# Kernel tuning notes

Hardware: AMD Instinct MI355X
Metric: run time of the kernel (lower is better)

## Reference

```python
import jax, jax.numpy as jnp
import numpy as np

START, STOP, T = 28, 29, 30

def _lstm_dir(x, h0, c0, w_ih, w_hh, b_ih, b_hh):
    # x: (S, B, E) -> hs: (S, B, H)
    xw = jnp.einsum('sbe,ge->sbg', x, w_ih) + b_ih + b_hh  # (S,B,4H)
    def step(carry, g_x):
        h, c = carry
        g = g_x + h @ w_hh.T
        i, f, gg, o = jnp.split(g, 4, axis=-1)
        c = jax.nn.sigmoid(f) * c + jax.nn.sigmoid(i) * jnp.tanh(gg)
        h = jax.nn.sigmoid(o) * jnp.tanh(c)
        return (h, c), h
    _, hs = jax.lax.scan(step, (h0, c0), xw)
    return hs

def setup_inputs() -> dict:
    key = jax.random.key(0)
    ks = jax.random.split(key, 16)
    S, B, V, E, H = 256, 32, 50000, 512, 512  # H = hidden_dim // 2
    d = {}
    d['sentence'] = jax.random.randint(ks[0], (S, B), 0, V)
    d['tags'] = jax.random.randint(ks[1], (S, B), 0, 28)
    d['emb'] = jax.random.normal(ks[2], (V, E), jnp.float32) * 0.1
    d['w_ih_f'] = jax.random.normal(ks[3], (4 * H, E), jnp.float32) * 0.05
    d['w_hh_f'] = jax.random.normal(ks[4], (4 * H, H), jnp.float32) * 0.05
    d['b_ih_f'] = jax.random.normal(ks[5], (4 * H,), jnp.float32) * 0.05
    d['b_hh_f'] = jax.random.normal(ks[6], (4 * H,), jnp.float32) * 0.05
    d['w_ih_b'] = jax.random.normal(ks[7], (4 * H, E), jnp.float32) * 0.05
    d['w_hh_b'] = jax.random.normal(ks[8], (4 * H, H), jnp.float32) * 0.05
    d['b_ih_b'] = jax.random.normal(ks[9], (4 * H,), jnp.float32) * 0.05
    d['b_hh_b'] = jax.random.normal(ks[10], (4 * H,), jnp.float32) * 0.05
    d['w_out'] = jax.random.normal(ks[11], (T, 2 * H), jnp.float32) * 0.05
    d['b_out'] = jax.random.normal(ks[12], (T,), jnp.float32) * 0.05
    tr = jax.random.normal(ks[13], (T, T), jnp.float32)
    tr = tr.at[START, :].set(-10000.0).at[:, STOP].set(-10000.0)
    d['transitions'] = tr
    d['h0'] = jax.random.normal(ks[14], (2, B, H), jnp.float32)
    d['c0'] = jax.random.normal(ks[15], (2, B, H), jnp.float32)
    return d

def reference(sentence, tags, emb, w_ih_f, w_hh_f, b_ih_f, b_hh_f,
              w_ih_b, w_hh_b, b_ih_b, b_hh_b, w_out, b_out, transitions, h0, c0):
    S, B = sentence.shape
    x = emb[sentence]                                   # (S,B,E)
    hf = _lstm_dir(x, h0[0], c0[0], w_ih_f, w_hh_f, b_ih_f, b_hh_f)
    hb = _lstm_dir(x[::-1], h0[1], c0[1], w_ih_b, w_hh_b, b_ih_b, b_hh_b)[::-1]
    lstm_out = jnp.concatenate([hf, hb], axis=-1)       # (S,B,2H)
    feats = jnp.einsum('sbh,th->bst', lstm_out, w_out) + b_out  # (B,S,T)

    # CRF partition function (forward algorithm)
    fv0 = jnp.full((B, T), -10000.0, feats.dtype).at[:, START].set(0.0)
    def crf_step(fv, feat):  # fv (B,T), feat (B,T)
        fv = jax.nn.logsumexp(fv[:, None, :] + transitions[None, :, :] + feat[:, :, None], axis=2)
        return fv, None
    fv, _ = jax.lax.scan(crf_step, fv0, feats.transpose(1, 0, 2))
    forward_score = jax.nn.logsumexp(fv + transitions[STOP][None, :], axis=1)  # (B,)

    # gold path score
    tags_b = tags.T                                     # (B,S)
    tags_ext = jnp.concatenate([jnp.full((B, 1), START, tags_b.dtype), tags_b], axis=1)  # (B,S+1)
    t_prev, t_next = tags_ext[:, :-1], tags_ext[:, 1:]
    trans_sc = transitions[t_next, t_prev].sum(axis=1)
    emit_sc = jnp.take_along_axis(feats, t_next[:, :, None], axis=2)[:, :, 0].sum(axis=1)
    gold_score = trans_sc + emit_sc + transitions[STOP, tags_ext[:, -1]]

    return jnp.sum(forward_score - gold_score)
```

## Files before the change

### kernel.cpp

```cpp
#include <hip/hip_runtime.h>
#include <hip/hip_bf16.h>
#include <math.h>

#define S_LEN 256
#define B 32
#define E 512
#define H 512
#define G4 2048
#define T_TAGS 30
#define START_TAG 28
#define STOP_TAG 29

typedef unsigned short u16;
typedef unsigned int   u32;
typedef unsigned long long u64;
typedef __attribute__((ext_vector_type(8))) short bf16x8;
typedef __attribute__((ext_vector_type(4))) float f32x4;

__device__ __forceinline__ float bf2f(u16 u){
  u32 x = ((u32)u) << 16;
  return __uint_as_float(x);
}
__device__ __forceinline__ u16 f2bf(float f){
  u32 x = __float_as_uint(f);
  u32 r = (x + 0x7fffu + ((x >> 16) & 1u)) >> 16;
  return (u16)r;
}
__device__ __forceinline__ float sigf(float x){
  return 1.0f / (1.0f + __expf(-x));
}
__device__ __forceinline__ float tanh_fast(float x){
  return 1.0f - 2.0f / (__expf(2.0f * x) + 1.0f);
}

__global__ __launch_bounds__(256) void k_prep_a(
    const int* __restrict__ sent, const float* __restrict__ emb,
    u16* __restrict__ a16)
{
  int g = (blockIdx.x * 256 + threadIdx.x) * 8;
  int token = g >> 9, k = g & 511;
  const float* src = emb + (size_t)sent[token] * E + k;
  float4 v0 = *reinterpret_cast<const float4*>(src);
  float4 v1 = *reinterpret_cast<const float4*>(src + 4);
  u16 o[8];
  o[0]=f2bf(v0.x); o[1]=f2bf(v0.y); o[2]=f2bf(v0.z); o[3]=f2bf(v0.w);
  o[4]=f2bf(v1.x); o[5]=f2bf(v1.y); o[6]=f2bf(v1.z); o[7]=f2bf(v1.w);
  *reinterpret_cast<uint4*>(a16 + g) = *reinterpret_cast<const uint4*>(o);
}

__global__ __launch_bounds__(256) void k_cvt(const float* __restrict__ src, u16* __restrict__ dst){
  int g = (blockIdx.x * 256 + threadIdx.x) * 8;
  float4 v0 = *reinterpret_cast<const float4*>(src + g);
  float4 v1 = *reinterpret_cast<const float4*>(src + g + 4);
  u16 o[8];
  o[0]=f2bf(v0.x); o[1]=f2bf(v0.y); o[2]=f2bf(v0.z); o[3]=f2bf(v0.w);
  o[4]=f2bf(v1.x); o[5]=f2bf(v1.y); o[6]=f2bf(v1.z); o[7]=f2bf(v1.w);
  *reinterpret_cast<uint4*>(dst + g) = *reinterpret_cast<const uint4*>(o);
}

__global__ __launch_bounds__(256) void k_init16(
    const float* __restrict__ h0, u16* __restrict__ h16, u32* __restrict__ bar)
{
  int g = (blockIdx.x * 256 + threadIdx.x) * 8;
  float4 v0 = *reinterpret_cast<const float4*>(h0 + g);
  float4 v1 = *reinterpret_cast<const float4*>(h0 + g + 4);
  u16 o[8];
  o[0]=f2bf(v0.x); o[1]=f2bf(v0.y); o[2]=f2bf(v0.z); o[3]=f2bf(v0.w);
  o[4]=f2bf(v1.x); o[5]=f2bf(v1.y); o[6]=f2bf(v1.z); o[7]=f2bf(v1.w);
  *reinterpret_cast<uint4*>(h16 + g) = *reinterpret_cast<const uint4*>(o);
  if (blockIdx.x == 0 && threadIdx.x < 64) bar[threadIdx.x] = 0u;
}

__global__ __launch_bounds__(256) void k_gemm_xw16(
    const u16* __restrict__ a16, const u16* __restrict__ w16ih,
    const float* __restrict__ b_ih_f, const float* __restrict__ b_hh_f,
    const float* __restrict__ b_ih_b, const float* __restrict__ b_hh_b,
    u16* __restrict__ xw)
{
  int dir = blockIdx.z;
  int n0 = blockIdx.x * 128;
  int m0 = blockIdx.y * 128;
  const u16* Wp = w16ih + (size_t)dir * G4 * E;
  const float* bi = dir ? b_ih_b : b_ih_f;
  const float* bh = dir ? b_hh_b : b_hh_f;
  int tid = threadIdx.x;

  __shared__ u16 As[128 * 32];
  __shared__ u16 Bs[128 * 32];

  int l  = tid & 63;
  int wid = tid >> 6;
  int wr = wid >> 1, wc = wid & 1;
  int lr = l & 15, lh = l >> 4;
  int swzr = (lh ^ (lr & 3)) << 3;

  f32x4 acc[4][4];
  #pragma unroll
  for (int i = 0; i < 4; ++i)
    #pragma unroll
    for (int j = 0; j < 4; ++j)
      acc[i][j] = (f32x4){0.f, 0.f, 0.f, 0.f};

  for (int kt = 0; kt < E; kt += 32){
    __syncthreads();
    #pragma unroll
    for (int it = 0; it < 2; ++it){
      int u = it * 256 + tid;
      int row = u >> 2, c = u & 3;
      int sw = (c ^ (row & 3)) << 3;
      *reinterpret_cast<uint4*>(&As[row * 32 + sw]) =
        *reinterpret_cast<const uint4*>(a16 + (size_t)(m0 + row) * E + kt + c * 8);
      *reinterpret_cast<uint4*>(&Bs[row * 32 + sw]) =
        *reinterpret_cast<const uint4*>(Wp + (size_t)(n0 + row) * E + kt + c * 8);
    }
    __syncthreads();
    bf16x8 a[4], b[4];
    #pragma unroll
    for (int mi = 0; mi < 4; ++mi)
      a[mi] = *reinterpret_cast<const bf16x8*>(&As[(wr * 64 + mi * 16 + lr) * 32 + swzr]);
    #pragma unroll
    for (int ni = 0; ni < 4; ++ni)
      b[ni] = *reinterpret_cast<const bf16x8*>(&Bs[(wc * 64 + ni * 16 + lr) * 32 + swzr]);
    #pragma unroll
    for (int mi = 0; mi < 4; ++mi)
      #pragma unroll
      for (int ni = 0; ni < 4; ++ni)
        acc[mi][ni] = __builtin_amdgcn_mfma_f32_16x16x32_bf16(a[mi], b[ni], acc[mi][ni], 0, 0, 0);
  }

  #pragma unroll
  for (int ni = 0; ni < 4; ++ni){
    int n = n0 + wc * 64 + ni * 16 + lr;
    float bias = bi[n] + bh[n];
    #pragma unroll
    for (int mi = 0; mi < 4; ++mi){
      #pragma unroll
      for (int r = 0; r < 4; ++r){
        int m = m0 + wr * 64 + mi * 16 + lh * 4 + r;
        xw[((size_t)dir * 8192 + m) * G4 + n] = f2bf(acc[mi][ni][r] + bias);
      }
    }
  }
}

__global__ __launch_bounds__(128) void k_lstm_fast(
    const float* __restrict__ w_hh_f, const float* __restrict__ w_hh_b,
    const u16* __restrict__ xw,
    u16* __restrict__ ht,
    const float* __restrict__ c0,
    u16* __restrict__ hseq,
    u32* __restrict__ bar)
{
  __shared__ u16 w_s[64 * 512];

  const int bx    = blockIdx.x;
  const int dir   = bx >> 5;
  const int slice = bx & 31;
  const int j0    = slice << 4;
  const int tid   = threadIdx.x;
  const int l     = tid & 63;
  const int wr    = tid >> 6;
  const int lr    = l & 15, lh = l >> 4;
  const int sw    = (lr & 7) << 3;

  const float* wsrc = dir ? w_hh_b : w_hh_f;
  #pragma unroll
  for (int i = 0; i < 32; ++i){
    int u = i * 128 + tid;
    int r = u >> 6, ku8 = u & 63;
    int g = r >> 4, jj = r & 15;
    const float* src = wsrc + (size_t)((g << 9) + j0 + jj) * H + ku8 * 8;
    float4 a = *reinterpret_cast<const float4*>(src);
    float4 b = *reinterpret_cast<const float4*>(src + 4);
    u16 o[8];
    o[0]=f2bf(a.x); o[1]=f2bf(a.y); o[2]=f2bf(a.z); o[3]=f2bf(a.w);
    o[4]=f2bf(b.x); o[5]=f2bf(b.y); o[6]=f2bf(b.z); o[7]=f2bf(b.w);
    int idx = (r * 512 + ku8 * 8) ^ ((r & 7) << 3);
    *reinterpret_cast<uint4*>(&w_s[idx]) = *reinterpret_cast<const uint4*>(o);
  }

  int bbase[4];
  #pragma unroll
  for (int G = 0; G < 4; ++G)
    bbase[G] = (G * 16 + lr) * 512 + (lh << 3);

  const int aoff = ((wr << 4) + lr) * 512 + (lh << 3);

  float c_reg[4];
  #pragma unroll
  for (int r = 0; r < 4; ++r)
    c_reg[r] = c0[((size_t)dir * B + (wr * 16 + lh * 4 + r)) * H + j0 + lr];

  const u32* flg = bar + (dir << 5);
  const int PSTRIDE = 2 * B * H;

  __syncthreads();

  for (int t = 0; t < S_LEN; ++t){
    const int s_eff = dir ? (S_LEN - 1 - t) : t;

    u16 xv[4][4];
    {
      const u16* xb = xw + ((size_t)dir * 8192 + (size_t)s_eff * B) * G4 + j0 + lr;
      #pragma unroll
      for (int r = 0; r < 4; ++r){
        const u16* xr = xb + (size_t)(wr * 16 + lh * 4 + r) * G4;
        #pragma unroll
        for (int G = 0; G < 4; ++G) xv[G][r] = xr[G << 9];
      }
    }

    {
      u32 f;
      do {
        f = __hip_atomic_load(flg + (l & 31), __ATOMIC_RELAXED, __HIP_MEMORY_SCOPE_AGENT);
      } while (__any(f < (u32)t));
    }

    const u64* hp = reinterpret_cast<const u64*>(
        ht + (size_t)(t & 1) * PSTRIDE + (size_t)dir * (B * H) + aoff);
    u64 qa[32];
    #pragma unroll
    for (int kt = 0; kt < 16; ++kt){
      qa[2*kt]   = __hip_atomic_load(hp + kt * 8,     __ATOMIC_RELAXED, __HIP_MEMORY_SCOPE_AGENT);
      qa[2*kt+1] = __hip_atomic_load(hp + kt * 8 + 1, __ATOMIC_RELAXED, __HIP_MEMORY_SCOPE_AGENT);
    }

    f32x4 acc[4];
    #pragma unroll
    for (int G = 0; G < 4; ++G) acc[G] = (f32x4){0.f, 0.f, 0.f, 0.f};
    #pragma unroll
    for (int kt = 0; kt < 16; ++kt){
      union { u64 q[2]; bf16x8 v; } ua;
      ua.q[0] = qa[2*kt]; ua.q[1] = qa[2*kt+1];
      #pragma unroll
      for (int G = 0; G < 4; ++G){
        bf16x8 bfr = *reinterpret_cast<const bf16x8*>(&w_s[(bbase[G] + (kt << 5)) ^ sw]);
        acc[G] = __builtin_amdgcn_mfma_f32_16x16x32_bf16(ua.v, bfr, acc[G], 0, 0, 0);
      }
    }

    u32 spack[4];
    #pragma unroll
    for (int r = 0; r < 4; ++r){
      float iv = acc[0][r] + bf2f(xv[0][r]);
      float fv = acc[1][r] + bf2f(xv[1][r]);
      float gv = acc[2][r] + bf2f(xv[2][r]);
      float ov = acc[3][r] + bf2f(xv[3][r]);
      float cn = sigf(fv) * c_reg[r] + sigf(iv) * tanh_fast(gv);
      float hv = sigf(ov) * tanh_fast(cn);
      c_reg[r] = cn;
      u32 hu = (u32)f2bf(hv);
      u32 po = (u32)__shfl_xor((int)hu, 1);
      u32 pack = hu | (po << 16);
      spack[r] = pack;
      if ((lr & 1) == 0){
        int batch = wr * 16 + lh * 4 + r;
        size_t off = ((size_t)dir * B + batch) * H + j0 + lr;
        __hip_atomic_store(
            reinterpret_cast<u32*>(ht + (size_t)((t + 1) & 1) * PSTRIDE + off),
            pack, __ATOMIC_RELAXED, __HIP_MEMORY_SCOPE_AGENT);
      }
    }

    asm volatile("s_waitcnt vmcnt(0)" ::: "memory");
    __syncthreads();
    if (tid == 0)
      __hip_atomic_store(bar + (dir << 5) + slice, (u32)(t + 1),
                         __ATOMIC_RELAXED, __HIP_MEMORY_SCOPE_AGENT);

    if ((lr & 1) == 0){
      #pragma unroll
      for (int r = 0; r < 4; ++r){
        int batch = wr * 16 + lh * 4 + r;
        *reinterpret_cast<u32*>(
            hseq + ((size_t)dir * 8192 + (size_t)s_eff * B + batch) * H + j0 + lr) = spack[r];
      }
    }
  }
}

__global__ __launch_bounds__(256) void k_feats2(
    const u16* __restrict__ hseq, const float* __restrict__ w_out,
    const float* __restrict__ b_out, float* __restrict__ feats)
{
  __shared__ float row[32][1028];
  int blk = blockIdx.x;
  int tid = threadIdx.x;
  const u16* hf16 = hseq;
  const u16* hb16 = hseq + (size_t)8192 * H;

  #pragma unroll
  for (int it = 0; it < 16; ++it){
    int u = it * 256 + tid;
    int flat = u * 8;
    int i = flat >> 10, d = flat & 1023;
    int m = blk * 32 + i;
    const u16* src = (d < 512) ? (hf16 + (size_t)m * H + d) : (hb16 + (size_t)m * H + d - 512);
    uint4 v = *reinterpret_cast<const uint4*>(src);
    float* dst = &row[i][d];
    dst[0] = bf2f((u16)(v.x & 0xffff)); dst[1] = bf2f((u16)(v.x >> 16));
    dst[2] = bf2f((u16)(v.y & 0xffff)); dst[3] = bf2f((u16)(v.y >> 16));
    dst[4] = bf2f((u16)(v.z & 0xffff)); dst[5] = bf2f((u16)(v.z >> 16));
    dst[6] = bf2f((u16)(v.w & 0xffff)); dst[7] = bf2f((u16)(v.w >> 16));
  }
  __syncthreads();

  int i = tid >> 3, tg = tid & 7;
  const float* w0 = w_out + (size_t)((tg + 0  < T_TAGS) ? tg + 0  : 0) * 1024;
  const float* w1 = w_out + (size_t)((tg + 8  < T_TAGS) ? tg + 8  : 0) * 1024;
  const float* w2 = w_out + (size_t)((tg + 16 < T_TAGS) ? tg + 16 : 0) * 1024;
  const float* w3 = w_out + (size_t)((tg + 24 < T_TAGS) ? tg + 24 : 0) * 1024;
  float s0 = 0.f, s1 = 0.f, s2 = 0.f, s3 = 0.f;
  #pragma unroll 4
  for (int k4 = 0; k4 < 256; ++k4){
    float4 rv = *reinterpret_cast<const float4*>(&row[i][k4 * 4]);
    float4 a = *reinterpret_cast<const float4*>(w0 + k4 * 4);
    float4 b = *reinterpret_cast<const float4*>(w1 + k4 * 4);
    float4 c = *reinterpret_cast<const float4*>(w2 + k4 * 4);
    float4 d = *reinterpret_cast<const float4*>(w3 + k4 * 4);
    s0 = fmaf(a.x,rv.x,s0); s0 = fmaf(a.y,rv.y,s0); s0 = fmaf(a.z,rv.z,s0); s0 = fmaf(a.w,rv.w,s0);
    s1 = fmaf(b.x,rv.x,s1); s1 = fmaf(b.y,rv.y,s1); s1 = fmaf(b.z,rv.z,s1); s1 = fmaf(b.w,rv.w,s1);
    s2 = fmaf(c.x,rv.x,s2); s2 = fmaf(c.y,rv.y,s2); s2 = fmaf(c.z,rv.z,s2); s2 = fmaf(c.w,rv.w,s2);
    s3 = fmaf(d.x,rv.x,s3); s3 = fmaf(d.y,rv.y,s3); s3 = fmaf(d.z,rv.z,s3); s3 = fmaf(d.w,rv.w,s3);
  }
  int m = blk * 32 + i;
  int s = m >> 5, bb = m & 31;
  float* fp = feats + ((size_t)bb * S_LEN + s) * T_TAGS;
  float sums[4] = {s0, s1, s2, s3};
  #pragma unroll
  for (int q = 0; q < 4; ++q){
    int tt = tg + q * 8;
    if (tt < T_TAGS) fp[tt] = sums[q] + b_out[tt];
  }
}

__global__ __launch_bounds__(64) void k_crf2(
    const float* __restrict__ feats, const float* __restrict__ trans,
    const int* __restrict__ tags, float* __restrict__ scores)
{
  int b = blockIdx.x;
  int l = threadIdx.x;

  float trr[T_TAGS];
  #pragma unroll
  for (int j = 0; j < T_TAGS; ++j)
    trr[j] = (l < T_TAGS) ? trans[l * T_TAGS + j] : -1e30f;

  float fv = (l == START_TAG) ? 0.f : -10000.f;
  const float* fb = feats + (size_t)b * S_LEN * T_TAGS;

  for (int s = 0; s < S_LEN; ++s){
    float feat = (l < T_TAGS) ? fb[s * T_TAGS + l] : 0.f;
    float v[T_TAGS];
    float m = -1e30f;
    #pragma unroll
    for (int j = 0; j < T_TAGS; ++j){
      float fvj = __shfl(fv, j);
      v[j] = fvj + trr[j];
      m = fmaxf(m, v[j]);
    }
    float sum = 0.f;
    #pragma unroll
    for (int j = 0; j < T_TAGS; ++j) sum += __expf(v[j] - m);
    fv = feat + m + __logf(sum);
  }

  float fin = (l < T_TAGS) ? fv + trans[STOP_TAG * T_TAGS + l] : -1e30f;
  float mm = fin;
  #pragma unroll
  for (int o = 32; o > 0; o >>= 1) mm = fmaxf(mm, __shfl_xor(mm, o));
  float e = (l < T_TAGS) ? __expf(fin - mm) : 0.f;
  #pragma unroll
  for (int o = 32; o > 0; o >>= 1) e += __shfl_xor(e, o);
  float fsc = mm + __logf(e);

  float g = 0.f;
  #pragma unroll
  for (int it = 0; it < 4; ++it){
    int s = it * 64 + l;
    int nxt = tags[s * B + b];
    int prv = s ? tags[(s - 1) * B + b] : START_TAG;
    g += trans[nxt * T_TAGS + prv] + fb[s * T_TAGS + nxt];
  }
  #pragma unroll
  for (int o = 32; o > 0; o >>= 1) g += __shfl_down(g, o);
  if (l == 0){
    int last = tags[(S_LEN - 1) * B + b];
    g += trans[STOP_TAG * T_TAGS + last];
    scores[b] = fsc - g;
  }
}

__global__ void k_final(const float* __restrict__ scores, float* __restrict__ out){
  int tid = threadIdx.x;
  float v = (tid < B) ? scores[tid] : 0.f;
  #pragma unroll
  for (int o = 32; o > 0; o >>= 1) v += __shfl_down(v, o);
  if (tid == 0) out[0] = v;
}

extern "C" void kernel_launch(void* const* d_in, const int* in_sizes, int n_in,
                              void* d_out, int out_size, void* d_ws, size_t ws_size,
                              hipStream_t stream)
{
  const int*   sent   = (const int*)d_in[0];
  const int*   tags   = (const int*)d_in[1];
  const float* emb    = (const float*)d_in[2];
  const float* w_ih_f = (const float*)d_in[3];
  const float* w_hh_f = (const float*)d_in[4];
  const float* b_ih_f = (const float*)d_in[5];
  const float* b_hh_f = (const float*)d_in[6];
  const float* w_ih_b = (const float*)d_in[7];
  const float* w_hh_b = (const float*)d_in[8];
  const float* b_ih_b = (const float*)d_in[9];
  const float* b_hh_b = (const float*)d_in[10];
  const float* w_out  = (const float*)d_in[11];
  const float* b_out  = (const float*)d_in[12];
  const float* trans  = (const float*)d_in[13];
  const float* h0     = (const float*)d_in[14];
  const float* c0     = (const float*)d_in[15];

  const size_t OFF_XW   = 0;
  const size_t OFF_A16  = 67108864;
  const size_t OFF_WIH  = 75497472;
  const size_t OFF_HSEQ = 79691776;
  const size_t OFF_HT   = 96468992;
  const size_t OFF_FEATS= 96600064;
  const size_t OFF_SC   = 97583104;
  const size_t OFF_BAR  = 97583232;
  const size_t NEED     = 97583488;
  if (ws_size < NEED) return;

  char* ws = (char*)d_ws;
  u16*   xw     = (u16*)(ws + OFF_XW);
  u16*   a16    = (u16*)(ws + OFF_A16);
  u16*   w16ih  = (u16*)(ws + OFF_WIH);
  u16*   hseq   = (u16*)(ws + OFF_HSEQ);
  u16*   ht     = (u16*)(ws + OFF_HT);
  float* feats  = (float*)(ws + OFF_FEATS);
  float* scores = (float*)(ws + OFF_SC);
  u32*   bar    = (u32*)(ws + OFF_BAR);

  k_prep_a<<<2048, 256, 0, stream>>>(sent, emb, a16);
  k_cvt<<<512, 256, 0, stream>>>(w_ih_f, w16ih);
  k_cvt<<<512, 256, 0, stream>>>(w_ih_b, w16ih + (size_t)G4 * E);
  k_init16<<<16, 256, 0, stream>>>(h0, ht, bar);

  k_gemm_xw16<<<dim3(G4 / 128, 8192 / 128, 2), 256, 0, stream>>>(
      a16, w16ih, b_ih_f, b_hh_f, b_ih_b, b_hh_b, xw);

  k_lstm_fast<<<64, 128, 0, stream>>>(w_hh_f, w_hh_b, xw, ht, c0, hseq, bar);

  k_feats2<<<256, 256, 0, stream>>>(hseq, w_out, b_out, feats);
  k_crf2<<<B, 64, 0, stream>>>(feats, trans, tags, scores);
  k_final<<<1, 64, 0, stream>>>(scores, (float*)d_out);
}
```

Before: 1.604 ms.

## Fuse input projection GEMM into the persistent LSTM recurrence kernel

Removes the standalone bf16 input-projection GEMM and the two weight-conversion kernels. Each persistent LSTM block now keeps its slice of W_ih in LDS next to W_hh and computes the next timestep's x·W_ih with MFMAs right after publishing h. That step's accumulator then seeds the recurrent matmul, and the bias is added in the epilogue. This drops the large xw intermediate (write plus per-step strided reads) and its launch. The cost is extra MFMA work and global A loads inside the serial step loop, plus doubled LDS use per block.

```diff
diff --git a/kernel.cpp b/kernel.cpp
--- a/kernel.cpp
+++ b/kernel.cpp
@@ -48,16 +48,6 @@
   *reinterpret_cast<uint4*>(a16 + g) = *reinterpret_cast<const uint4*>(o);
 }
 
-__global__ __launch_bounds__(256) void k_cvt(const float* __restrict__ src, u16* __restrict__ dst){
-  int g = (blockIdx.x * 256 + threadIdx.x) * 8;
-  float4 v0 = *reinterpret_cast<const float4*>(src + g);
-  float4 v1 = *reinterpret_cast<const float4*>(src + g + 4);
-  u16 o[8];
-  o[0]=f2bf(v0.x); o[1]=f2bf(v0.y); o[2]=f2bf(v0.z); o[3]=f2bf(v0.w);
-  o[4]=f2bf(v1.x); o[5]=f2bf(v1.y); o[6]=f2bf(v1.z); o[7]=f2bf(v1.w);
-  *reinterpret_cast<uint4*>(dst + g) = *reinterpret_cast<const uint4*>(o);
-}
-
 __global__ __launch_bounds__(256) void k_init16(
     const float* __restrict__ h0, u16* __restrict__ h16, u32* __restrict__ bar)
 {
@@ -71,87 +61,43 @@
   if (blockIdx.x == 0 && threadIdx.x < 64) bar[threadIdx.x] = 0u;
 }
 
-__global__ __launch_bounds__(256) void k_gemm_xw16(
-    const u16* __restrict__ a16, const u16* __restrict__ w16ih,
+__device__ __forceinline__ void compute_xw(
+    const u64* __restrict__ ap, const u16* __restrict__ wih_s,
+    const int* __restrict__ bbase, int sw, f32x4* __restrict__ xacc)
+{
+  u64 qb[32];
+  #pragma unroll
+  for (int kt = 0; kt < 16; ++kt){
+    qb[2*kt]   = ap[kt * 8];
+    qb[2*kt+1] = ap[kt * 8 + 1];
+  }
+  #pragma unroll
+  for (int G = 0; G < 4; ++G) xacc[G] = (f32x4){0.f, 0.f, 0.f, 0.f};
+  #pragma unroll
+  for (int kt = 0; kt < 16; ++kt){
+    union { u64 q[2]; bf16x8 v; } ua;
+    ua.q[0] = qb[2*kt]; ua.q[1] = qb[2*kt+1];
+    #pragma unroll
+    for (int G = 0; G < 4; ++G){
+      bf16x8 bfr = *reinterpret_cast<const bf16x8*>(&wih_s[(bbase[G] + (kt << 5)) ^ sw]);
+      xacc[G] = __builtin_amdgcn_mfma_f32_16x16x32_bf16(ua.v, bfr, xacc[G], 0, 0, 0);
+    }
+  }
+}
+
+__global__ __launch_bounds__(128) void k_lstm_fused(
+    const float* __restrict__ w_hh_f, const float* __restrict__ w_hh_b,
+    const float* __restrict__ w_ih_f, const float* __restrict__ w_ih_b,
     const float* __restrict__ b_ih_f, const float* __restrict__ b_hh_f,
     const float* __restrict__ b_ih_b, const float* __restrict__ b_hh_b,
-    u16* __restrict__ xw)
-{
-  int dir = blockIdx.z;
-  int n0 = blockIdx.x * 128;
-  int m0 = blockIdx.y * 128;
-  const u16* Wp = w16ih + (size_t)dir * G4 * E;
-  const float* bi = dir ? b_ih_b : b_ih_f;
-  const float* bh = dir ? b_hh_b : b_hh_f;
-  int tid = threadIdx.x;
-
-  __shared__ u16 As[128 * 32];
-  __shared__ u16 Bs[128 * 32];
-
-  int l  = tid & 63;
-  int wid = tid >> 6;
-  int wr = wid >> 1, wc = wid & 1;
-  int lr = l & 15, lh = l >> 4;
-  int swzr = (lh ^ (lr & 3)) << 3;
-
-  f32x4 acc[4][4];
-  #pragma unroll
-  for (int i = 0; i < 4; ++i)
-    #pragma unroll
-    for (int j = 0; j < 4; ++j)
-      acc[i][j] = (f32x4){0.f, 0.f, 0.f, 0.f};
-
-  for (int kt = 0; kt < E; kt += 32){
-    __syncthreads();
-    #pragma unroll
-    for (int it = 0; it < 2; ++it){
-      int u = it * 256 + tid;
-      int row = u >> 2, c = u & 3;
-      int sw = (c ^ (row & 3)) << 3;
-      *reinterpret_cast<uint4*>(&As[row * 32 + sw]) =
-        *reinterpret_cast<const uint4*>(a16 + (size_t)(m0 + row) * E + kt + c * 8);
-      *reinterpret_cast<uint4*>(&Bs[row * 32 + sw]) =
-        *reinterpret_cast<const uint4*>(Wp + (size_t)(n0 + row) * E + kt + c * 8);
-    }
-    __syncthreads();
-    bf16x8 a[4], b[4];
-    #pragma unroll
-    for (int mi = 0; mi < 4; ++mi)
-      a[mi] = *reinterpret_cast<const bf16x8*>(&As[(wr * 64 + mi * 16 + lr) * 32 + swzr]);
-    #pragma unroll
-    for (int ni = 0; ni < 4; ++ni)
-      b[ni] = *reinterpret_cast<const bf16x8*>(&Bs[(wc * 64 + ni * 16 + lr) * 32 + swzr]);
-    #pragma unroll
-    for (int mi = 0; mi < 4; ++mi)
-      #pragma unroll
-      for (int ni = 0; ni < 4; ++ni)
-        acc[mi][ni] = __builtin_amdgcn_mfma_f32_16x16x32_bf16(a[mi], b[ni], acc[mi][ni], 0, 0, 0);
-  }
-
-  #pragma unroll
-  for (int ni = 0; ni < 4; ++ni){
-    int n = n0 + wc * 64 + ni * 16 + lr;
-    float bias = bi[n] + bh[n];
-    #pragma unroll
-    for (int mi = 0; mi < 4; ++mi){
-      #pragma unroll
-      for (int r = 0; r < 4; ++r){
-        int m = m0 + wr * 64 + mi * 16 + lh * 4 + r;
-        xw[((size_t)dir * 8192 + m) * G4 + n] = f2bf(acc[mi][ni][r] + bias);
-      }
-    }
-  }
-}
-
-__global__ __launch_bounds__(128) void k_lstm_fast(
-    const float* __restrict__ w_hh_f, const float* __restrict__ w_hh_b,
-    const u16* __restrict__ xw,
+    const u16* __restrict__ a16,
     u16* __restrict__ ht,
     const float* __restrict__ c0,
     u16* __restrict__ hseq,
     u32* __restrict__ bar)
 {
-  __shared__ u16 w_s[64 * 512];
+  __shared__ u16 whh_s[64 * 512];
+  __shared__ u16 wih_s[64 * 512];
 
   const int bx    = blockIdx.x;
   const int dir   = bx >> 5;
@@ -163,20 +109,33 @@
   const int lr    = l & 15, lh = l >> 4;
   const int sw    = (lr & 7) << 3;
 
-  const float* wsrc = dir ? w_hh_b : w_hh_f;
-  #pragma unroll
-  for (int i = 0; i < 32; ++i){
-    int u = i * 128 + tid;
-    int r = u >> 6, ku8 = u & 63;
-    int g = r >> 4, jj = r & 15;
-    const float* src = wsrc + (size_t)((g << 9) + j0 + jj) * H + ku8 * 8;
-    float4 a = *reinterpret_cast<const float4*>(src);
-    float4 b = *reinterpret_cast<const float4*>(src + 4);
-    u16 o[8];
-    o[0]=f2bf(a.x); o[1]=f2bf(a.y); o[2]=f2bf(a.z); o[3]=f2bf(a.w);
-    o[4]=f2bf(b.x); o[5]=f2bf(b.y); o[6]=f2bf(b.z); o[7]=f2bf(b.w);
-    int idx = (r * 512 + ku8 * 8) ^ ((r & 7) << 3);
-    *reinterpret_cast<uint4*>(&w_s[idx]) = *reinterpret_cast<const uint4*>(o);
+  {
+    const float* hsrc = dir ? w_hh_b : w_hh_f;
+    const float* isrc = dir ? w_ih_b : w_ih_f;
+    #pragma unroll
+    for (int i = 0; i < 32; ++i){
+      int u = i * 128 + tid;
+      int r = u >> 6, ku8 = u & 63;
+      int g = r >> 4, jj = r & 15;
+      size_t roff = (size_t)((g << 9) + j0 + jj) * H + ku8 * 8;
+      int idx = (r * 512 + ku8 * 8) ^ ((r & 7) << 3);
+      {
+        float4 a = *reinterpret_cast<const float4*>(hsrc + roff);
+        float4 b = *reinterpret_cast<const float4*>(hsrc + roff + 4);
+        u16 o[8];
+        o[0]=f2bf(a.x); o[1]=f2bf(a.y); o[2]=f2bf(a.z); o[3]=f2bf(a.w);
+        o[4]=f2bf(b.x); o[5]=f2bf(b.y); o[6]=f2bf(b.z); o[7]=f2bf(b.w);
+        *reinterpret_cast<uint4*>(&whh_s[idx]) = *reinterpret_cast<const uint4*>(o);
+      }
+      {
+        float4 a = *reinterpret_cast<const float4*>(isrc + roff);
+        float4 b = *reinterpret_cast<const float4*>(isrc + roff + 4);
+        u16 o[8];
+        o[0]=f2bf(a.x); o[1]=f2bf(a.y); o[2]=f2bf(a.z); o[3]=f2bf(a.w);
+        o[4]=f2bf(b.x); o[5]=f2bf(b.y); o[6]=f2bf(b.z); o[7]=f2bf(b.w);
+        *reinterpret_cast<uint4*>(&wih_s[idx]) = *reinterpret_cast<const uint4*>(o);
+      }
+    }
   }
 
   int bbase[4];
@@ -186,6 +145,15 @@
 
   const int aoff = ((wr << 4) + lr) * 512 + (lh << 3);
 
+  float bias_g[4];
+  {
+    const float* bi = dir ? b_ih_b : b_ih_f;
+    const float* bh = dir ? b_hh_b : b_hh_f;
+    #pragma unroll
+    for (int G = 0; G < 4; ++G)
+      bias_g[G] = bi[(G << 9) + j0 + lr] + bh[(G << 9) + j0 + lr];
+  }
+
   float c_reg[4];
   #pragma unroll
   for (int r = 0; r < 4; ++r)
@@ -196,19 +164,16 @@
 
   __syncthreads();
 
+  f32x4 xacc[4];
+  {
+    int s0 = dir ? (S_LEN - 1) : 0;
+    const u64* ap = reinterpret_cast<const u64*>(
+        a16 + ((size_t)(s0 * B + wr * 16 + lr)) * 512 + (lh << 3));
+    compute_xw(ap, wih_s, bbase, sw, xacc);
+  }
+
   for (int t = 0; t < S_LEN; ++t){
     const int s_eff = dir ? (S_LEN - 1 - t) : t;
-
-    u16 xv[4][4];
-    {
-      const u16* xb = xw + ((size_t)dir * 8192 + (size_t)s_eff * B) * G4 + j0 + lr;
-      #pragma unroll
-      for (int r = 0; r < 4; ++r){
-        const u16* xr = xb + (size_t)(wr * 16 + lh * 4 + r) * G4;
-        #pragma unroll
-        for (int G = 0; G < 4; ++G) xv[G][r] = xr[G << 9];
-      }
-    }
 
     {
       u32 f;
@@ -228,14 +193,14 @@
 
     f32x4 acc[4];
     #pragma unroll
-    for (int G = 0; G < 4; ++G) acc[G] = (f32x4){0.f, 0.f, 0.f, 0.f};
+    for (int G = 0; G < 4; ++G) acc[G] = xacc[G];
     #pragma unroll
     for (int kt = 0; kt < 16; ++kt){
       union { u64 q[2]; bf16x8 v; } ua;
       ua.q[0] = qa[2*kt]; ua.q[1] = qa[2*kt+1];
       #pragma unroll
       for (int G = 0; G < 4; ++G){
-        bf16x8 bfr = *reinterpret_cast<const bf16x8*>(&w_s[(bbase[G] + (kt << 5)) ^ sw]);
+        bf16x8 bfr = *reinterpret_cast<const bf16x8*>(&whh_s[(bbase[G] + (kt << 5)) ^ sw]);
         acc[G] = __builtin_amdgcn_mfma_f32_16x16x32_bf16(ua.v, bfr, acc[G], 0, 0, 0);
       }
     }
@@ -243,10 +208,10 @@
     u32 spack[4];
     #pragma unroll
     for (int r = 0; r < 4; ++r){
-      float iv = acc[0][r] + bf2f(xv[0][r]);
-      float fv = acc[1][r] + bf2f(xv[1][r]);
-      float gv = acc[2][r] + bf2f(xv[2][r]);
-      float ov = acc[3][r] + bf2f(xv[3][r]);
+      float iv = acc[0][r] + bias_g[0];
+      float fv = acc[1][r] + bias_g[1];
+      float gv = acc[2][r] + bias_g[2];
+      float ov = acc[3][r] + bias_g[3];
       float cn = sigf(fv) * c_reg[r] + sigf(iv) * tanh_fast(gv);
       float hv = sigf(ov) * tanh_fast(cn);
       c_reg[r] = cn;
@@ -276,6 +241,13 @@
         *reinterpret_cast<u32*>(
             hseq + ((size_t)dir * 8192 + (size_t)s_eff * B + batch) * H + j0 + lr) = spack[r];
       }
+    }
+
+    if (t < S_LEN - 1){
+      int s_next = dir ? (S_LEN - 2 - t) : (t + 1);
+      const u64* ap = reinterpret_cast<const u64*>(
+          a16 + ((size_t)(s_next * B + wr * 16 + lr)) * 512 + (lh << 3));
+      compute_xw(ap, wih_s, bbase, sw, xacc);
     }
   }
 }
@@ -421,21 +393,17 @@
   const float* h0     = (const float*)d_in[14];
   const float* c0     = (const float*)d_in[15];
 
-  const size_t OFF_XW   = 0;
-  const size_t OFF_A16  = 67108864;
-  const size_t OFF_WIH  = 75497472;
-  const size_t OFF_HSEQ = 79691776;
-  const size_t OFF_HT   = 96468992;
-  const size_t OFF_FEATS= 96600064;
-  const size_t OFF_SC   = 97583104;
-  const size_t OFF_BAR  = 97583232;
-  const size_t NEED     = 97583488;
+  const size_t OFF_A16  = 0;
+  const size_t OFF_HSEQ = 8388608;
+  const size_t OFF_HT   = 25165824;
+  const size_t OFF_FEATS= 25296896;
+  const size_t OFF_SC   = 26279936;
+  const size_t OFF_BAR  = 26280064;
+  const size_t NEED     = 26280320;
   if (ws_size < NEED) return;
 
   char* ws = (char*)d_ws;
-  u16*   xw     = (u16*)(ws + OFF_XW);
   u16*   a16    = (u16*)(ws + OFF_A16);
-  u16*   w16ih  = (u16*)(ws + OFF_WIH);
   u16*   hseq   = (u16*)(ws + OFF_HSEQ);
   u16*   ht     = (u16*)(ws + OFF_HT);
   float* feats  = (float*)(ws + OFF_FEATS);
@@ -443,14 +411,12 @@
   u32*   bar    = (u32*)(ws + OFF_BAR);
 
   k_prep_a<<<2048, 256, 0, stream>>>(sent, emb, a16);
-  k_cvt<<<512, 256, 0, stream>>>(w_ih_f, w16ih);
-  k_cvt<<<512, 256, 0, stream>>>(w_ih_b, w16ih + (size_t)G4 * E);
   k_init16<<<16, 256, 0, stream>>>(h0, ht, bar);
 
-  k_gemm_xw16<<<dim3(G4 / 128, 8192 / 128, 2), 256, 0, stream>>>(
-      a16, w16ih, b_ih_f, b_hh_f, b_ih_b, b_hh_b, xw);
-
-  k_lstm_fast<<<64, 128, 0, stream>>>(w_hh_f, w_hh_b, xw, ht, c0, hseq, bar);
+  k_lstm_fused<<<64, 128, 0, stream>>>(
+      w_hh_f, w_hh_b, w_ih_f, w_ih_b,
+      b_ih_f, b_hh_f, b_ih_b, b_hh_b,
+      a16, ht, c0, hseq, bar);
 
   k_feats2<<<256, 256, 0, stream>>>(hseq, w_out, b_out, feats);
   k_crf2<<<B, 64, 0, stream>>>(feats, trans, tags, scores);
```

Result: slower. 2.015 ms (+25.6%).

## Fuse input-projection GEMM with LSTM recurrence in a persistent producer-consumer kernel

Applied to the files above, without the earlier changes.

Merges the embedding gather, fp32-to-bf16 conversion, input-projection GEMM and the recurrent LSTM into one launch. 64 blocks run the recurrence while 192 worker blocks compute xw tiles in time order, publishing per-tile flags that the LSTM blocks poll before loading each step's gate inputs. The GEMM runs concurrently with the serial recurrence instead of before it, and the separate conversion kernels and their intermediate buffers are removed. In exchange it relies on all 256 blocks being co-resident to avoid deadlock, converts operands on every GEMM tile load, and leaves half the LSTM block's waves idle.

```diff
diff --git a/kernel.cpp b/kernel.cpp
--- a/kernel.cpp
+++ b/kernel.cpp
@@ -10,6 +10,8 @@
 #define T_TAGS 30
 #define START_TAG 28
 #define STOP_TAG 29
+#define NWORK 192
+#define NTILE 2048
 
 typedef unsigned short u16;
 typedef unsigned int   u32;
@@ -31,31 +33,6 @@
 }
 __device__ __forceinline__ float tanh_fast(float x){
   return 1.0f - 2.0f / (__expf(2.0f * x) + 1.0f);
-}
-
-__global__ __launch_bounds__(256) void k_prep_a(
-    const int* __restrict__ sent, const float* __restrict__ emb,
-    u16* __restrict__ a16)
-{
-  int g = (blockIdx.x * 256 + threadIdx.x) * 8;
-  int token = g >> 9, k = g & 511;
-  const float* src = emb + (size_t)sent[token] * E + k;
-  float4 v0 = *reinterpret_cast<const float4*>(src);
-  float4 v1 = *reinterpret_cast<const float4*>(src + 4);
-  u16 o[8];
-  o[0]=f2bf(v0.x); o[1]=f2bf(v0.y); o[2]=f2bf(v0.z); o[3]=f2bf(v0.w);
-  o[4]=f2bf(v1.x); o[5]=f2bf(v1.y); o[6]=f2bf(v1.z); o[7]=f2bf(v1.w);
-  *reinterpret_cast<uint4*>(a16 + g) = *reinterpret_cast<const uint4*>(o);
-}
-
-__global__ __launch_bounds__(256) void k_cvt(const float* __restrict__ src, u16* __restrict__ dst){
-  int g = (blockIdx.x * 256 + threadIdx.x) * 8;
-  float4 v0 = *reinterpret_cast<const float4*>(src + g);
-  float4 v1 = *reinterpret_cast<const float4*>(src + g + 4);
-  u16 o[8];
-  o[0]=f2bf(v0.x); o[1]=f2bf(v0.y); o[2]=f2bf(v0.z); o[3]=f2bf(v0.w);
-  o[4]=f2bf(v1.x); o[5]=f2bf(v1.y); o[6]=f2bf(v1.z); o[7]=f2bf(v1.w);
-  *reinterpret_cast<uint4*>(dst + g) = *reinterpret_cast<const uint4*>(o);
 }
 
 __global__ __launch_bounds__(256) void k_init16(
@@ -68,214 +45,286 @@
   o[0]=f2bf(v0.x); o[1]=f2bf(v0.y); o[2]=f2bf(v0.z); o[3]=f2bf(v0.w);
   o[4]=f2bf(v1.x); o[5]=f2bf(v1.y); o[6]=f2bf(v1.z); o[7]=f2bf(v1.w);
   *reinterpret_cast<uint4*>(h16 + g) = *reinterpret_cast<const uint4*>(o);
-  if (blockIdx.x == 0 && threadIdx.x < 64) bar[threadIdx.x] = 0u;
-}
-
-__global__ __launch_bounds__(256) void k_gemm_xw16(
-    const u16* __restrict__ a16, const u16* __restrict__ w16ih,
+  if (blockIdx.x == 0 && threadIdx.x < 192) bar[threadIdx.x] = 0u;
+}
+
+__global__ __launch_bounds__(256) void k_mega(
+    const int* __restrict__ sent, const float* __restrict__ emb,
+    const float* __restrict__ w_ih_f, const float* __restrict__ w_ih_b,
+    const float* __restrict__ w_hh_f, const float* __restrict__ w_hh_b,
     const float* __restrict__ b_ih_f, const float* __restrict__ b_hh_f,
     const float* __restrict__ b_ih_b, const float* __restrict__ b_hh_b,
-    u16* __restrict__ xw)
-{
-  int dir = blockIdx.z;
-  int n0 = blockIdx.x * 128;
-  int m0 = blockIdx.y * 128;
-  const u16* Wp = w16ih + (size_t)dir * G4 * E;
-  const float* bi = dir ? b_ih_b : b_ih_f;
-  const float* bh = dir ? b_hh_b : b_hh_f;
-  int tid = threadIdx.x;
-
-  __shared__ u16 As[128 * 32];
-  __shared__ u16 Bs[128 * 32];
-
-  int l  = tid & 63;
-  int wid = tid >> 6;
-  int wr = wid >> 1, wc = wid & 1;
-  int lr = l & 15, lh = l >> 4;
-  int swzr = (lh ^ (lr & 3)) << 3;
-
-  f32x4 acc[4][4];
-  #pragma unroll
-  for (int i = 0; i < 4; ++i)
-    #pragma unroll
-    for (int j = 0; j < 4; ++j)
-      acc[i][j] = (f32x4){0.f, 0.f, 0.f, 0.f};
-
-  for (int kt = 0; kt < E; kt += 32){
-    __syncthreads();
-    #pragma unroll
-    for (int it = 0; it < 2; ++it){
-      int u = it * 256 + tid;
-      int row = u >> 2, c = u & 3;
-      int sw = (c ^ (row & 3)) << 3;
-      *reinterpret_cast<uint4*>(&As[row * 32 + sw]) =
-        *reinterpret_cast<const uint4*>(a16 + (size_t)(m0 + row) * E + kt + c * 8);
-      *reinterpret_cast<uint4*>(&Bs[row * 32 + sw]) =
-        *reinterpret_cast<const uint4*>(Wp + (size_t)(n0 + row) * E + kt + c * 8);
-    }
-    __syncthreads();
-    bf16x8 a[4], b[4];
-    #pragma unroll
-    for (int mi = 0; mi < 4; ++mi)
-      a[mi] = *reinterpret_cast<const bf16x8*>(&As[(wr * 64 + mi * 16 + lr) * 32 + swzr]);
-    #pragma unroll
-    for (int ni = 0; ni < 4; ++ni)
-      b[ni] = *reinterpret_cast<const bf16x8*>(&Bs[(wc * 64 + ni * 16 + lr) * 32 + swzr]);
-    #pragma unroll
-    for (int mi = 0; mi < 4; ++mi)
-      #pragma unroll
-      for (int ni = 0; ni < 4; ++ni)
-        acc[mi][ni] = __builtin_amdgcn_mfma_f32_16x16x32_bf16(a[mi], b[ni], acc[mi][ni], 0, 0, 0);
-  }
-
-  #pragma unroll
-  for (int ni = 0; ni < 4; ++ni){
-    int n = n0 + wc * 64 + ni * 16 + lr;
-    float bias = bi[n] + bh[n];
-    #pragma unroll
-    for (int mi = 0; mi < 4; ++mi){
-      #pragma unroll
-      for (int r = 0; r < 4; ++r){
-        int m = m0 + wr * 64 + mi * 16 + lh * 4 + r;
-        xw[((size_t)dir * 8192 + m) * G4 + n] = f2bf(acc[mi][ni][r] + bias);
-      }
-    }
-  }
-}
-
-__global__ __launch_bounds__(128) void k_lstm_fast(
-    const float* __restrict__ w_hh_f, const float* __restrict__ w_hh_b,
-    const u16* __restrict__ xw,
+    u16* __restrict__ xw,
     u16* __restrict__ ht,
     const float* __restrict__ c0,
     u16* __restrict__ hseq,
     u32* __restrict__ bar)
 {
-  __shared__ u16 w_s[64 * 512];
-
-  const int bx    = blockIdx.x;
-  const int dir   = bx >> 5;
-  const int slice = bx & 31;
-  const int j0    = slice << 4;
-  const int tid   = threadIdx.x;
-  const int l     = tid & 63;
-  const int wr    = tid >> 6;
-  const int lr    = l & 15, lh = l >> 4;
-  const int sw    = (lr & 7) << 3;
-
-  const float* wsrc = dir ? w_hh_b : w_hh_f;
-  #pragma unroll
-  for (int i = 0; i < 32; ++i){
-    int u = i * 128 + tid;
-    int r = u >> 6, ku8 = u & 63;
-    int g = r >> 4, jj = r & 15;
-    const float* src = wsrc + (size_t)((g << 9) + j0 + jj) * H + ku8 * 8;
-    float4 a = *reinterpret_cast<const float4*>(src);
-    float4 b = *reinterpret_cast<const float4*>(src + 4);
-    u16 o[8];
-    o[0]=f2bf(a.x); o[1]=f2bf(a.y); o[2]=f2bf(a.z); o[3]=f2bf(a.w);
-    o[4]=f2bf(b.x); o[5]=f2bf(b.y); o[6]=f2bf(b.z); o[7]=f2bf(b.w);
-    int idx = (r * 512 + ku8 * 8) ^ ((r & 7) << 3);
-    *reinterpret_cast<uint4*>(&w_s[idx]) = *reinterpret_cast<const uint4*>(o);
-  }
-
-  int bbase[4];
-  #pragma unroll
-  for (int G = 0; G < 4; ++G)
-    bbase[G] = (G * 16 + lr) * 512 + (lh << 3);
-
-  const int aoff = ((wr << 4) + lr) * 512 + (lh << 3);
-
-  float c_reg[4];
-  #pragma unroll
-  for (int r = 0; r < 4; ++r)
-    c_reg[r] = c0[((size_t)dir * B + (wr * 16 + lh * 4 + r)) * H + j0 + lr];
-
-  const u32* flg = bar + (dir << 5);
-  const int PSTRIDE = 2 * B * H;
-
-  __syncthreads();
-
-  for (int t = 0; t < S_LEN; ++t){
-    const int s_eff = dir ? (S_LEN - 1 - t) : t;
-
-    u16 xv[4][4];
+  __shared__ u16 pool[64 * 512];
+  __shared__ int toks[128];
+
+  const int tid = threadIdx.x;
+  u32* lstm_flg = bar;
+  u32* xw_flg   = bar + 64;
+
+  if (blockIdx.x < 64){
+    const int bx    = blockIdx.x;
+    const int dir   = bx >> 5;
+    const int slice = bx & 31;
+    const int j0    = slice << 4;
+    u16* w_s = pool;
+
     {
-      const u16* xb = xw + ((size_t)dir * 8192 + (size_t)s_eff * B) * G4 + j0 + lr;
+      const float* wsrc = dir ? w_hh_b : w_hh_f;
       #pragma unroll
-      for (int r = 0; r < 4; ++r){
-        const u16* xr = xb + (size_t)(wr * 16 + lh * 4 + r) * G4;
-        #pragma unroll
-        for (int G = 0; G < 4; ++G) xv[G][r] = xr[G << 9];
+      for (int i = 0; i < 16; ++i){
+        int u = i * 256 + tid;
+        int r = u >> 6, ku8 = u & 63;
+        int g = r >> 4, jj = r & 15;
+        const float* src = wsrc + (size_t)((g << 9) + j0 + jj) * H + ku8 * 8;
+        float4 a = *reinterpret_cast<const float4*>(src);
+        float4 b = *reinterpret_cast<const float4*>(src + 4);
+        u16 o[8];
+        o[0]=f2bf(a.x); o[1]=f2bf(a.y); o[2]=f2bf(a.z); o[3]=f2bf(a.w);
+        o[4]=f2bf(b.x); o[5]=f2bf(b.y); o[6]=f2bf(b.z); o[7]=f2bf(b.w);
+        int idx = (r * 512 + ku8 * 8) ^ ((r & 7) << 3);
+        *reinterpret_cast<uint4*>(&w_s[idx]) = *reinterpret_cast<const uint4*>(o);
       }
     }
 
-    {
+    const int l  = tid & 63;
+    const int wv = tid >> 6;
+    const int wr = wv & 1;
+    const int lr = l & 15, lh = l >> 4;
+    const int sw = (lr & 7) << 3;
+
+    int bbase[4];
+    #pragma unroll
+    for (int G = 0; G < 4; ++G)
+      bbase[G] = (G * 16 + lr) * 512 + (lh << 3);
+    const int aoff = ((wr << 4) + lr) * 512 + (lh << 3);
+
+    float c_reg[4];
+    if (wv < 2){
+      #pragma unroll
+      for (int r = 0; r < 4; ++r)
+        c_reg[r] = c0[((size_t)dir * B + (wr * 16 + lh * 4 + r)) * H + j0 + lr];
+    }
+
+    const u32* flg = lstm_flg + (dir << 5);
+    const int PSTRIDE = 2 * B * H;
+    const u32* xw32 = reinterpret_cast<const u32*>(xw);
+    const int lrE = lr & ~1, half = lr & 1;
+
+    __syncthreads();
+
+    u32 xq[16];
+    if (wv < 2){
+      int s0 = dir ? (S_LEN - 1) : 0;
+      int mt = s0 >> 2;
       u32 f;
       do {
-        f = __hip_atomic_load(flg + (l & 31), __ATOMIC_RELAXED, __HIP_MEMORY_SCOPE_AGENT);
-      } while (__any(f < (u32)t));
+        f = __hip_atomic_load(xw_flg + (dir << 6) + mt, __ATOMIC_RELAXED, __HIP_MEMORY_SCOPE_AGENT);
+      } while (__any(f < 16u));
+      size_t base = ((size_t)dir * 8192 + (size_t)s0 * B) * G4;
+      #pragma unroll
+      for (int G = 0; G < 4; ++G)
+        #pragma unroll
+        for (int r = 0; r < 4; ++r){
+          size_t eidx = base + (size_t)(wr * 16 + lh * 4 + r) * G4 + (G << 9) + j0 + lrE;
+          xq[G * 4 + r] = __hip_atomic_load(xw32 + (eidx >> 1),
+                            __ATOMIC_RELAXED, __HIP_MEMORY_SCOPE_AGENT);
+        }
     }
-
-    const u64* hp = reinterpret_cast<const u64*>(
-        ht + (size_t)(t & 1) * PSTRIDE + (size_t)dir * (B * H) + aoff);
-    u64 qa[32];
-    #pragma unroll
-    for (int kt = 0; kt < 16; ++kt){
-      qa[2*kt]   = __hip_atomic_load(hp + kt * 8,     __ATOMIC_RELAXED, __HIP_MEMORY_SCOPE_AGENT);
-      qa[2*kt+1] = __hip_atomic_load(hp + kt * 8 + 1, __ATOMIC_RELAXED, __HIP_MEMORY_SCOPE_AGENT);
-    }
-
-    f32x4 acc[4];
-    #pragma unroll
-    for (int G = 0; G < 4; ++G) acc[G] = (f32x4){0.f, 0.f, 0.f, 0.f};
-    #pragma unroll
-    for (int kt = 0; kt < 16; ++kt){
-      union { u64 q[2]; bf16x8 v; } ua;
-      ua.q[0] = qa[2*kt]; ua.q[1] = qa[2*kt+1];
-      #pragma unroll
-      for (int G = 0; G < 4; ++G){
-        bf16x8 bfr = *reinterpret_cast<const bf16x8*>(&w_s[(bbase[G] + (kt << 5)) ^ sw]);
-        acc[G] = __builtin_amdgcn_mfma_f32_16x16x32_bf16(ua.v, bfr, acc[G], 0, 0, 0);
+    int mt_ready = dir ? 63 : 0;
+
+    for (int t = 0; t < S_LEN; ++t){
+      const int s_eff = dir ? (S_LEN - 1 - t) : t;
+      u32 spack[4];
+
+      if (wv < 2){
+        {
+          u32 f;
+          do {
+            f = __hip_atomic_load(flg + (l & 31), __ATOMIC_RELAXED, __HIP_MEMORY_SCOPE_AGENT);
+          } while (__any(f < (u32)t));
+        }
+
+        const u64* hp = reinterpret_cast<const u64*>(
+            ht + (size_t)(t & 1) * PSTRIDE + (size_t)dir * (B * H) + aoff);
+        u64 qa[32];
+        #pragma unroll
+        for (int kt = 0; kt < 16; ++kt){
+          qa[2*kt]   = __hip_atomic_load(hp + kt * 8,     __ATOMIC_RELAXED, __HIP_MEMORY_SCOPE_AGENT);
+          qa[2*kt+1] = __hip_atomic_load(hp + kt * 8 + 1, __ATOMIC_RELAXED, __HIP_MEMORY_SCOPE_AGENT);
+        }
+
+        f32x4 acc[4];
+        #pragma unroll
+        for (int G = 0; G < 4; ++G) acc[G] = (f32x4){0.f, 0.f, 0.f, 0.f};
+        #pragma unroll
+        for (int kt = 0; kt < 16; ++kt){
+          union { u64 q[2]; bf16x8 v; } ua;
+          ua.q[0] = qa[2*kt]; ua.q[1] = qa[2*kt+1];
+          #pragma unroll
+          for (int G = 0; G < 4; ++G){
+            bf16x8 bfr = *reinterpret_cast<const bf16x8*>(&w_s[(bbase[G] + (kt << 5)) ^ sw]);
+            acc[G] = __builtin_amdgcn_mfma_f32_16x16x32_bf16(ua.v, bfr, acc[G], 0, 0, 0);
+          }
+        }
+
+        #pragma unroll
+        for (int r = 0; r < 4; ++r){
+          float iv = acc[0][r] + bf2f((u16)(xq[0*4+r] >> (16*half)));
+          float fv = acc[1][r] + bf2f((u16)(xq[1*4+r] >> (16*half)));
+          float gv = acc[2][r] + bf2f((u16)(xq[2*4+r] >> (16*half)));
+          float ov = acc[3][r] + bf2f((u16)(xq[3*4+r] >> (16*half)));
+          float cn = sigf(fv) * c_reg[r] + sigf(iv) * tanh_fast(gv);
+          float hv = sigf(ov) * tanh_fast(cn);
+          c_reg[r] = cn;
+          u32 hu = (u32)f2bf(hv);
+          u32 po = (u32)__shfl_xor((int)hu, 1);
+          u32 pack = hu | (po << 16);
+          spack[r] = pack;
+          if ((lr & 1) == 0){
+            int batch = wr * 16 + lh * 4 + r;
+            size_t off = ((size_t)dir * B + batch) * H + j0 + lr;
+            __hip_atomic_store(
+                reinterpret_cast<u32*>(ht + (size_t)((t + 1) & 1) * PSTRIDE + off),
+                pack, __ATOMIC_RELAXED, __HIP_MEMORY_SCOPE_AGENT);
+          }
+        }
+      }
+
+      asm volatile("s_waitcnt vmcnt(0)" ::: "memory");
+      __syncthreads();
+      if (tid == 0)
+        __hip_atomic_store(lstm_flg + (dir << 5) + slice, (u32)(t + 1),
+                           __ATOMIC_RELAXED, __HIP_MEMORY_SCOPE_AGENT);
+
+      if (wv < 2){
+        if ((lr & 1) == 0){
+          #pragma unroll
+          for (int r = 0; r < 4; ++r){
+            int batch = wr * 16 + lh * 4 + r;
+            *reinterpret_cast<u32*>(
+                hseq + ((size_t)dir * 8192 + (size_t)s_eff * B + batch) * H + j0 + lr) = spack[r];
+          }
+        }
+        if (t < S_LEN - 1){
+          int s_next = dir ? (S_LEN - 2 - t) : (t + 1);
+          int mt = s_next >> 2;
+          if (mt != mt_ready){
+            u32 f;
+            do {
+              f = __hip_atomic_load(xw_flg + (dir << 6) + mt, __ATOMIC_RELAXED, __HIP_MEMORY_SCOPE_AGENT);
+            } while (__any(f < 16u));
+            mt_ready = mt;
+          }
+          size_t base = ((size_t)dir * 8192 + (size_t)s_next * B) * G4;
+          #pragma unroll
+          for (int G = 0; G < 4; ++G)
+            #pragma unroll
+            for (int r = 0; r < 4; ++r){
+              size_t eidx = base + (size_t)(wr * 16 + lh * 4 + r) * G4 + (G << 9) + j0 + lrE;
+              xq[G * 4 + r] = __hip_atomic_load(xw32 + (eidx >> 1),
+                                __ATOMIC_RELAXED, __HIP_MEMORY_SCOPE_AGENT);
+            }
+        }
       }
     }
-
-    u32 spack[4];
-    #pragma unroll
-    for (int r = 0; r < 4; ++r){
-      float iv = acc[0][r] + bf2f(xv[0][r]);
-      float fv = acc[1][r] + bf2f(xv[1][r]);
-      float gv = acc[2][r] + bf2f(xv[2][r]);
-      float ov = acc[3][r] + bf2f(xv[3][r]);
-      float cn = sigf(fv) * c_reg[r] + sigf(iv) * tanh_fast(gv);
-      float hv = sigf(ov) * tanh_fast(cn);
-      c_reg[r] = cn;
-      u32 hu = (u32)f2bf(hv);
-      u32 po = (u32)__shfl_xor((int)hu, 1);
-      u32 pack = hu | (po << 16);
-      spack[r] = pack;
-      if ((lr & 1) == 0){
-        int batch = wr * 16 + lh * 4 + r;
-        size_t off = ((size_t)dir * B + batch) * H + j0 + lr;
-        __hip_atomic_store(
-            reinterpret_cast<u32*>(ht + (size_t)((t + 1) & 1) * PSTRIDE + off),
-            pack, __ATOMIC_RELAXED, __HIP_MEMORY_SCOPE_AGENT);
+  } else {
+    const int worker = blockIdx.x - 64;
+    u16* As = pool;
+    u16* Bs = pool + 4096;
+
+    const int l  = tid & 63;
+    const int wid = tid >> 6;
+    const int wr = wid >> 1, wc = wid & 1;
+    const int lr = l & 15, lh = l >> 4;
+    const int swzr = (lh ^ (lr & 3)) << 3;
+
+    for (int idx = worker; idx < NTILE; idx += NWORK){
+      const int dir  = idx & 1;
+      const int k    = idx >> 1;
+      const int mt_o = k >> 4, nt = k & 15;
+      const int mt   = dir ? (63 - mt_o) : mt_o;
+      const int m0   = mt << 7, n0 = nt << 7;
+      const float* Wp = dir ? w_ih_b : w_ih_f;
+      const float* bi = dir ? b_ih_b : b_ih_f;
+      const float* bh = dir ? b_hh_b : b_hh_f;
+
+      __syncthreads();
+      if (tid < 128) toks[tid] = sent[m0 + tid];
+
+      f32x4 acc[4][4];
+      #pragma unroll
+      for (int i = 0; i < 4; ++i)
+        #pragma unroll
+        for (int j = 0; j < 4; ++j)
+          acc[i][j] = (f32x4){0.f, 0.f, 0.f, 0.f};
+
+      for (int kt = 0; kt < E; kt += 32){
+        __syncthreads();
+        #pragma unroll
+        for (int it = 0; it < 4; ++it){
+          int a = it * 256 + tid;
+          int row = a >> 3, q = a & 7;
+          int c = q >> 1, hf = q & 1;
+          int idxe = row * 32 + ((c ^ (row & 3)) << 3) + hf * 4;
+          {
+            const float* src = emb + (size_t)toks[row] * E + kt + q * 4;
+            float4 v = *reinterpret_cast<const float4*>(src);
+            u16 o[4] = {f2bf(v.x), f2bf(v.y), f2bf(v.z), f2bf(v.w)};
+            *reinterpret_cast<u64*>(&As[idxe]) = *reinterpret_cast<const u64*>(o);
+          }
+          {
+            const float* src = Wp + (size_t)(n0 + row) * E + kt + q * 4;
+            float4 v = *reinterpret_cast<const float4*>(src);
+            u16 o[4] = {f2bf(v.x), f2bf(v.y), f2bf(v.z), f2bf(v.w)};
+            *reinterpret_cast<u64*>(&Bs[idxe]) = *reinterpret_cast<const u64*>(o);
+          }
+        }
+        __syncthreads();
+        bf16x8 a[4], b[4];
+        #pragma unroll
+        for (int mi = 0; mi < 4; ++mi)
+          a[mi] = *reinterpret_cast<const bf16x8*>(&As[(wr * 64 + mi * 16 + lr) * 32 + swzr]);
+        #pragma unroll
+        for (int ni = 0; ni < 4; ++ni)
+          b[ni] = *reinterpret_cast<const bf16x8*>(&Bs[(wc * 64 + ni * 16 + lr) * 32 + swzr]);
+        #pragma unroll
+        for (int mi = 0; mi < 4; ++mi)
+          #pragma unroll
+          for (int ni = 0; ni < 4; ++ni)
+            acc[mi][ni] = __builtin_amdgcn_mfma_f32_16x16x32_bf16(a[mi], b[ni], acc[mi][ni], 0, 0, 0);
       }
-    }
-
-    asm volatile("s_waitcnt vmcnt(0)" ::: "memory");
-    __syncthreads();
-    if (tid == 0)
-      __hip_atomic_store(bar + (dir << 5) + slice, (u32)(t + 1),
-                         __ATOMIC_RELAXED, __HIP_MEMORY_SCOPE_AGENT);
-
-    if ((lr & 1) == 0){
+
       #pragma unroll
-      for (int r = 0; r < 4; ++r){
-        int batch = wr * 16 + lh * 4 + r;
-        *reinterpret_cast<u32*>(
-            hseq + ((size_t)dir * 8192 + (size_t)s_eff * B + batch) * H + j0 + lr) = spack[r];
+      for (int ni = 0; ni < 4; ++ni){
+        int n = n0 + wc * 64 + ni * 16 + lr;
+        float bias = bi[n] + bh[n];
+        #pragma unroll
+        for (int mi = 0; mi < 4; ++mi){
+          #pragma unroll
+          for (int r = 0; r < 4; ++r){
+            int m = m0 + wr * 64 + mi * 16 + lh * 4 + r;
+            u16 val = f2bf(acc[mi][ni][r] + bias);
+            u32 po = (u32)__shfl_xor((int)(u32)val, 1);
+            if ((lr & 1) == 0){
+              u32 pack = (u32)val | (po << 16);
+              size_t eidx = ((size_t)dir * 8192 + m) * G4 + n;
+              __hip_atomic_store(reinterpret_cast<u32*>(xw) + (eidx >> 1),
+                                 pack, __ATOMIC_RELAXED, __HIP_MEMORY_SCOPE_AGENT);
+            }
+          }
+        }
       }
+      asm volatile("s_waitcnt vmcnt(0)" ::: "memory");
+      __syncthreads();
+      if (tid == 0)
+        __hip_atomic_fetch_add(xw_flg + (dir << 6) + mt, 1u,
+                               __ATOMIC_RELAXED, __HIP_MEMORY_SCOPE_AGENT);
     }
   }
 }
@@ -422,35 +471,28 @@
   const float* c0     = (const float*)d_in[15];
 
   const size_t OFF_XW   = 0;
-  const size_t OFF_A16  = 67108864;
-  const size_t OFF_WIH  = 75497472;
-  const size_t OFF_HSEQ = 79691776;
-  const size_t OFF_HT   = 96468992;
-  const size_t OFF_FEATS= 96600064;
-  const size_t OFF_SC   = 97583104;
-  const size_t OFF_BAR  = 97583232;
-  const size_t NEED     = 97583488;
+  const size_t OFF_HSEQ = 67108864;
+  const size_t OFF_HT   = 83886080;
+  const size_t OFF_FEATS= 84017152;
+  const size_t OFF_SC   = 85000192;
+  const size_t OFF_BAR  = 85000320;
+  const size_t NEED     = 85001088;
   if (ws_size < NEED) return;
 
   char* ws = (char*)d_ws;
   u16*   xw     = (u16*)(ws + OFF_XW);
-  u16*   a16    = (u16*)(ws + OFF_A16);
-  u16*   w16ih  = (u16*)(ws + OFF_WIH);
   u16*   hseq   = (u16*)(ws + OFF_HSEQ);
   u16*   ht     = (u16*)(ws + OFF_HT);
   float* feats  = (float*)(ws + OFF_FEATS);
   float* scores = (float*)(ws + OFF_SC);
   u32*   bar    = (u32*)(ws + OFF_BAR);
 
-  k_prep_a<<<2048, 256, 0, stream>>>(sent, emb, a16);
-  k_cvt<<<512, 256, 0, stream>>>(w_ih_f, w16ih);
-  k_cvt<<<512, 256, 0, stream>>>(w_ih_b, w16ih + (size_t)G4 * E);
   k_init16<<<16, 256, 0, stream>>>(h0, ht, bar);
 
-  k_gemm_xw16<<<dim3(G4 / 128, 8192 / 128, 2), 256, 0, stream>>>(
-      a16, w16ih, b_ih_f, b_hh_f, b_ih_b, b_hh_b, xw);
-
-  k_lstm_fast<<<64, 128, 0, stream>>>(w_hh_f, w_hh_b, xw, ht, c0, hseq, bar);
+  k_mega<<<64 + NWORK, 256, 0, stream>>>(
+      sent, emb, w_ih_f, w_ih_b, w_hh_f, w_hh_b,
+      b_ih_f, b_hh_f, b_ih_b, b_hh_b,
+      xw, ht, c0, hseq, bar);
 
   k_feats2<<<256, 256, 0, stream>>>(hseq, w_out, b_out, feats);
   k_crf2<<<B, 64, 0, stream>>>(feats, trans, tags, scores);
```

After: 1.523 ms. -5.0%, faster.
